# Kernel tuning notes

Hardware: AMD Instinct MI355X
Metric: run time of the kernel (lower is better)

## Reference

```python
import jax, jax.numpy as jnp
import numpy as np

N_ENTITIES = 100000
N_USERS = 50000
N_FACTORS = 4
N_RELATIONS = 32
N_META = 8
CHANNEL = 64
N_EDGES = 1600000
NNZ = 1000000


def setup_inputs() -> dict:
    key = jax.random.key(0)
    ks = jax.random.split(key, 12)
    return {
        "entity_emb": jax.random.normal(ks[0], (N_ENTITIES, CHANNEL), jnp.float32) * 0.1,
        "user_emb": jax.random.normal(ks[1], (N_USERS, CHANNEL), jnp.float32) * 0.1,
        "latent_emb": jax.random.normal(ks[2], (N_FACTORS, CHANNEL), jnp.float32) * 0.1,
        "head": jax.random.randint(ks[3], (N_EDGES,), 0, N_ENTITIES, jnp.int32),
        "tail": jax.random.randint(ks[4], (N_EDGES,), 0, N_ENTITIES, jnp.int32),
        # edge_type values in [1, n_relations) so edge_type - 1 indexes (n_relations-1) rows
        "edge_type": jax.random.randint(ks[5], (N_EDGES,), 1, N_RELATIONS, jnp.int32),
        "mat_row": jax.random.randint(ks[6], (NNZ,), 0, N_USERS, jnp.int32),
        "mat_col": jax.random.randint(ks[7], (NNZ,), 0, N_ENTITIES, jnp.int32),
        "mat_val": jax.random.uniform(ks[8], (NNZ,), jnp.float32),
        "relation_edge_weight": jax.random.normal(ks[9], (N_RELATIONS - 1, CHANNEL), jnp.float32) * 0.1,
        "weight": jax.random.normal(ks[10], (N_META, CHANNEL), jnp.float32) * 0.1,
        "disen_weight_att": jax.random.normal(ks[11], (N_FACTORS, N_META), jnp.float32) * 0.1,
    }


def reference(entity_emb, user_emb, latent_emb, head, tail, edge_type,
              mat_row, mat_col, mat_val, relation_edge_weight, weight,
              disen_weight_att):
    n_entities, channel = entity_emb.shape
    n_users = user_emb.shape[0]

    # --- KG aggregation: GATED_ATT + INDEPENDENT_RELATION_EMB branch ---
    edge_rel = relation_edge_weight[edge_type - 1]                     # (E, C)
    att = jax.nn.sigmoid(jnp.sum(entity_emb[head] * edge_rel, axis=1)) # (E,)
    neigh = att[:, None] * (entity_emb[tail] * edge_rel)               # (E, C)
    seg_sum = jax.ops.segment_sum(neigh, head, num_segments=n_entities)
    cnt = jax.ops.segment_sum(jnp.ones((head.shape[0],), entity_emb.dtype),
                              head, num_segments=n_entities)
    entity_agg = seg_sum / jnp.maximum(cnt, 1.0)[:, None]              # scatter_mean

    # --- user aggregation ---
    score = jax.nn.softmax(user_emb @ latent_emb.T, axis=1)[:, :, None]  # (U, F, 1)
    # sparse mm: interact_mat (U x N_ent, COO) @ entity_emb
    user_agg = jax.ops.segment_sum(mat_val[:, None] * entity_emb[mat_col],
                                   mat_row, num_segments=n_users)        # (U, C)
    disen_weight = jax.nn.softmax(disen_weight_att, axis=-1) @ weight    # (F, C)
    user_agg = user_agg * (disen_weight[None, :, :] * score).sum(axis=1) + user_agg
    return entity_agg, user_agg
```

## Files before the change

kernel.cpp:

```cpp
#include <hip/hip_runtime.h>

constexpr int N_ENTITIES = 100000;
constexpr int N_USERS    = 50000;
constexpr int N_FACTORS  = 4;
constexpr int N_META     = 8;
constexpr int CHANNEL    = 64;
constexpr int N_EDGES    = 1600000;
constexpr int NNZ        = 1000000;

__device__ __forceinline__ float wave_reduce_sum(float v) {
    for (int off = 32; off > 0; off >>= 1)
        v += __shfl_xor(v, off, 64);
    return v;
}

__global__ void edge_kernel(const float* __restrict__ entity_emb,
                            const int*   __restrict__ head,
                            const int*   __restrict__ tail,
                            const int*   __restrict__ etype,
                            const float* __restrict__ rel_w,
                            float*       __restrict__ ent_acc,
                            float*       __restrict__ cnt) {
    const int lane = threadIdx.x & 63;
    const int wid  = (blockIdx.x * blockDim.x + threadIdx.x) >> 6;
    const int nw   = (gridDim.x * blockDim.x) >> 6;
    for (int e = wid; e < N_EDGES; e += nw) {
        const int h = head[e];
        const int t = tail[e];
        const int r = etype[e] - 1;
        const float rw = rel_w[r * CHANNEL + lane];
        const float eh = entity_emb[h * CHANNEL + lane];
        const float dot = wave_reduce_sum(eh * rw);
        const float att = 1.0f / (1.0f + expf(-dot));
        const float et  = entity_emb[t * CHANNEL + lane];
        atomicAdd(&ent_acc[h * CHANNEL + lane], att * et * rw);
        if (lane == 0) atomicAdd(&cnt[h], 1.0f);
    }
}

__global__ void spmm_kernel(const float* __restrict__ entity_emb,
                            const int*   __restrict__ mat_row,
                            const int*   __restrict__ mat_col,
                            const float* __restrict__ mat_val,
                            float*       __restrict__ user_acc) {
    const int lane = threadIdx.x & 63;
    const int wid  = (blockIdx.x * blockDim.x + threadIdx.x) >> 6;
    const int nw   = (gridDim.x * blockDim.x) >> 6;
    for (int i = wid; i < NNZ; i += nw) {
        const int r   = mat_row[i];
        const int c   = mat_col[i];
        const float v = mat_val[i];
        const float e = entity_emb[c * CHANNEL + lane];
        atomicAdd(&user_acc[r * CHANNEL + lane], v * e);
    }
}

__global__ void ent_final_kernel(float* __restrict__ ent,
                                 const float* __restrict__ cnt) {
    const int total = N_ENTITIES * (CHANNEL / 4);
    for (int i = blockIdx.x * blockDim.x + threadIdx.x; i < total;
         i += gridDim.x * blockDim.x) {
        const int row = i >> 4;
        const float inv = 1.0f / fmaxf(cnt[row], 1.0f);
        float4 v = reinterpret_cast<float4*>(ent)[i];
        v.x *= inv; v.y *= inv; v.z *= inv; v.w *= inv;
        reinterpret_cast<float4*>(ent)[i] = v;
    }
}

__global__ void user_final_kernel(const float* __restrict__ user_emb,
                                  const float* __restrict__ latent_emb,
                                  const float* __restrict__ weight,
                                  const float* __restrict__ datt,
                                  float*       __restrict__ user_out) {
    __shared__ float dw[N_FACTORS][CHANNEL];
    const int tid = threadIdx.x;
    if (tid < N_FACTORS * CHANNEL) {
        const int f = tid >> 6, c = tid & 63;
        float m = -1e30f;
        for (int j = 0; j < N_META; ++j) m = fmaxf(m, datt[f * N_META + j]);
        float p[N_META]; float s = 0.0f;
        for (int j = 0; j < N_META; ++j) { p[j] = expf(datt[f * N_META + j] - m); s += p[j]; }
        const float invs = 1.0f / s;
        float acc = 0.0f;
        for (int j = 0; j < N_META; ++j) acc += p[j] * invs * weight[j * CHANNEL + c];
        dw[f][c] = acc;
    }
    __syncthreads();

    const int lane = tid & 63;
    const int wib  = tid >> 6;
    const int wpb  = blockDim.x >> 6;
    for (int u = blockIdx.x * wpb + wib; u < N_USERS; u += gridDim.x * wpb) {
        const float ue = user_emb[u * CHANNEL + lane];
        float d0 = wave_reduce_sum(ue * latent_emb[0 * CHANNEL + lane]);
        float d1 = wave_reduce_sum(ue * latent_emb[1 * CHANNEL + lane]);
        float d2 = wave_reduce_sum(ue * latent_emb[2 * CHANNEL + lane]);
        float d3 = wave_reduce_sum(ue * latent_emb[3 * CHANNEL + lane]);
        const float m = fmaxf(fmaxf(d0, d1), fmaxf(d2, d3));
        d0 = expf(d0 - m); d1 = expf(d1 - m); d2 = expf(d2 - m); d3 = expf(d3 - m);
        const float invs = 1.0f / (d0 + d1 + d2 + d3);
        const float g = (d0 * dw[0][lane] + d1 * dw[1][lane] +
                         d2 * dw[2][lane] + d3 * dw[3][lane]) * invs;
        const float a = user_out[u * CHANNEL + lane];
        user_out[u * CHANNEL + lane] = a * (1.0f + g);
    }
}

extern "C" void kernel_launch(void* const* d_in, const int* in_sizes, int n_in,
                              void* d_out, int out_size, void* d_ws, size_t ws_size,
                              hipStream_t stream) {
    const float* entity_emb = (const float*)d_in[0];
    const float* user_emb   = (const float*)d_in[1];
    const float* latent_emb = (const float*)d_in[2];
    const int*   head       = (const int*)d_in[3];
    const int*   tail       = (const int*)d_in[4];
    const int*   etype      = (const int*)d_in[5];
    const int*   mat_row    = (const int*)d_in[6];
    const int*   mat_col    = (const int*)d_in[7];
    const float* mat_val    = (const float*)d_in[8];
    const float* rel_w      = (const float*)d_in[9];
    const float* weight     = (const float*)d_in[10];
    const float* datt       = (const float*)d_in[11];

    float* out      = (float*)d_out;
    float* ent_acc  = out;
    float* user_acc = out + (size_t)N_ENTITIES * CHANNEL;
    float* cnt      = (float*)d_ws;

    hipMemsetAsync(d_out, 0, (size_t)out_size * sizeof(float), stream);
    hipMemsetAsync(d_ws, 0, (size_t)N_ENTITIES * sizeof(float), stream);

    edge_kernel<<<4096, 256, 0, stream>>>(entity_emb, head, tail, etype, rel_w,
                                          ent_acc, cnt);
    spmm_kernel<<<4096, 256, 0, stream>>>(entity_emb, mat_row, mat_col, mat_val,
                                          user_acc);
    ent_final_kernel<<<2048, 256, 0, stream>>>(ent_acc, cnt);
    user_final_kernel<<<1024, 256, 0, stream>>>(user_emb, latent_emb, weight,
                                                datt, user_acc);
}
```

Measured before the change: 769.7 us.

## Replace atomic scatter aggregation with counting-sort CSR gather per entity and user

Builds CSR groupings of KG edges by head and of interaction nonzeros by user via count, scan, and scatter kernels, then computes each output row with one wave gathering its neighbors. This removes per-channel float atomics, output memsets and separate finalization passes, fusing the mean and user gating into the gather kernels. It adds index-sort passes with integer atomics and a serial single-block scan, and relies on a large workspace and on bit-packing tail and relation into one int.

```diff
diff --git a/kernel.cpp b/kernel.cpp
--- a/kernel.cpp
+++ b/kernel.cpp
@@ -7,6 +7,8 @@
 constexpr int CHANNEL    = 64;
 constexpr int N_EDGES    = 1600000;
 constexpr int NNZ        = 1000000;
+constexpr int N_REL      = 31;
+
 
 __device__ __forceinline__ float wave_reduce_sum(float v) {
     for (int off = 32; off > 0; off >>= 1)
@@ -14,65 +16,114 @@
     return v;
 }
 
-__global__ void edge_kernel(const float* __restrict__ entity_emb,
-                            const int*   __restrict__ head,
-                            const int*   __restrict__ tail,
-                            const int*   __restrict__ etype,
-                            const float* __restrict__ rel_w,
-                            float*       __restrict__ ent_acc,
-                            float*       __restrict__ cnt) {
-    const int lane = threadIdx.x & 63;
-    const int wid  = (blockIdx.x * blockDim.x + threadIdx.x) >> 6;
-    const int nw   = (gridDim.x * blockDim.x) >> 6;
-    for (int e = wid; e < N_EDGES; e += nw) {
+__global__ void count_kernel(const int* __restrict__ head,
+                             const int* __restrict__ mat_row,
+                             int* __restrict__ ent_cnt,
+                             int* __restrict__ user_cnt) {
+    const int i0 = blockIdx.x * blockDim.x + threadIdx.x;
+    const int stride = gridDim.x * blockDim.x;
+    for (int e = i0; e < N_EDGES; e += stride)
+        atomicAdd(&ent_cnt[head[e]], 1);
+    for (int z = i0; z < NNZ; z += stride)
+        atomicAdd(&user_cnt[mat_row[z]], 1);
+}
+
+__global__ void scan_kernel(const int* __restrict__ ent_cnt, int* __restrict__ ent_cur,
+                            const int* __restrict__ user_cnt, int* __restrict__ user_cur) {
+    const int* cnt = (blockIdx.x == 0) ? ent_cnt : user_cnt;
+    int*       cur = (blockIdx.x == 0) ? ent_cur : user_cur;
+    const int  n   = (blockIdx.x == 0) ? N_ENTITIES : N_USERS;
+    __shared__ int partial[1024];
+    const int per   = (n + 1023) >> 10;
+    const int start = threadIdx.x * per;
+    const int end   = min(start + per, n);
+    int s = 0;
+    for (int i = start; i < end; ++i) s += cnt[i];
+    partial[threadIdx.x] = s;
+    __syncthreads();
+    for (int d = 1; d < 1024; d <<= 1) {
+        int v = (threadIdx.x >= d) ? partial[threadIdx.x - d] : 0;
+        __syncthreads();
+        partial[threadIdx.x] += v;
+        __syncthreads();
+    }
+    int base = (threadIdx.x == 0) ? 0 : partial[threadIdx.x - 1];
+    for (int i = start; i < end; ++i) {
+        cur[i] = base;
+        base += cnt[i];
+    }
+}
+
+__global__ void scatter_kernel(const int* __restrict__ head,
+                               const int* __restrict__ tail,
+                               const int* __restrict__ etype,
+                               const int* __restrict__ mat_row,
+                               const int* __restrict__ mat_col,
+                               const float* __restrict__ mat_val,
+                               int* __restrict__ ent_cur,
+                               int* __restrict__ user_cur,
+                               int* __restrict__ edge_pl,
+                               int* __restrict__ nnz_col,
+                               float* __restrict__ nnz_val) {
+    const int i0 = blockIdx.x * blockDim.x + threadIdx.x;
+    const int stride = gridDim.x * blockDim.x;
+    for (int e = i0; e < N_EDGES; e += stride) {
         const int h = head[e];
-        const int t = tail[e];
-        const int r = etype[e] - 1;
-        const float rw = rel_w[r * CHANNEL + lane];
-        const float eh = entity_emb[h * CHANNEL + lane];
-        const float dot = wave_reduce_sum(eh * rw);
-        const float att = 1.0f / (1.0f + expf(-dot));
-        const float et  = entity_emb[t * CHANNEL + lane];
-        atomicAdd(&ent_acc[h * CHANNEL + lane], att * et * rw);
-        if (lane == 0) atomicAdd(&cnt[h], 1.0f);
-    }
-}
-
-__global__ void spmm_kernel(const float* __restrict__ entity_emb,
-                            const int*   __restrict__ mat_row,
-                            const int*   __restrict__ mat_col,
-                            const float* __restrict__ mat_val,
-                            float*       __restrict__ user_acc) {
-    const int lane = threadIdx.x & 63;
-    const int wid  = (blockIdx.x * blockDim.x + threadIdx.x) >> 6;
-    const int nw   = (gridDim.x * blockDim.x) >> 6;
-    for (int i = wid; i < NNZ; i += nw) {
-        const int r   = mat_row[i];
-        const int c   = mat_col[i];
-        const float v = mat_val[i];
-        const float e = entity_emb[c * CHANNEL + lane];
-        atomicAdd(&user_acc[r * CHANNEL + lane], v * e);
-    }
-}
-
-__global__ void ent_final_kernel(float* __restrict__ ent,
-                                 const float* __restrict__ cnt) {
-    const int total = N_ENTITIES * (CHANNEL / 4);
-    for (int i = blockIdx.x * blockDim.x + threadIdx.x; i < total;
-         i += gridDim.x * blockDim.x) {
-        const int row = i >> 4;
-        const float inv = 1.0f / fmaxf(cnt[row], 1.0f);
-        float4 v = reinterpret_cast<float4*>(ent)[i];
-        v.x *= inv; v.y *= inv; v.z *= inv; v.w *= inv;
-        reinterpret_cast<float4*>(ent)[i] = v;
-    }
-}
-
-__global__ void user_final_kernel(const float* __restrict__ user_emb,
-                                  const float* __restrict__ latent_emb,
-                                  const float* __restrict__ weight,
-                                  const float* __restrict__ datt,
-                                  float*       __restrict__ user_out) {
+        const int pos = atomicAdd(&ent_cur[h], 1);
+        edge_pl[pos] = tail[e] | ((etype[e] - 1) << 17);
+    }
+    for (int z = i0; z < NNZ; z += stride) {
+        const int r = mat_row[z];
+        const int pos = atomicAdd(&user_cur[r], 1);
+        nnz_col[pos] = mat_col[z];
+        nnz_val[pos] = mat_val[z];
+    }
+}
+
+__global__ void ent_agg_kernel(const float* __restrict__ entity_emb,
+                               const float* __restrict__ rel_w,
+                               const int* __restrict__ ent_cnt,
+                               const int* __restrict__ ent_cur,
+                               const int* __restrict__ edge_pl,
+                               float* __restrict__ out_ent) {
+    __shared__ float rw_s[N_REL][CHANNEL];
+    const int tid = threadIdx.x;
+    for (int i = tid; i < N_REL * CHANNEL; i += blockDim.x)
+        rw_s[i >> 6][i & 63] = rel_w[i];
+    __syncthreads();
+
+    const int lane = tid & 63;
+    const int wib  = tid >> 6;
+    const int wpb  = blockDim.x >> 6;
+    for (int h = blockIdx.x * wpb + wib; h < N_ENTITIES; h += gridDim.x * wpb) {
+        const int cnt   = ent_cnt[h];
+        const int end   = ent_cur[h];
+        const int start = end - cnt;
+        const float eh  = entity_emb[h * CHANNEL + lane];
+        float acc = 0.0f;
+        for (int i = start; i < end; ++i) {
+            const int pl = edge_pl[i];
+            const int t  = pl & 0x1FFFF;
+            const int r  = pl >> 17;
+            const float rw = rw_s[r][lane];
+            const float d  = wave_reduce_sum(eh * rw);
+            const float att = 1.0f / (1.0f + __expf(-d));
+            acc += att * rw * entity_emb[t * CHANNEL + lane];
+        }
+        out_ent[h * CHANNEL + lane] = acc / fmaxf((float)cnt, 1.0f);
+    }
+}
+
+__global__ void user_agg_kernel(const float* __restrict__ entity_emb,
+                                const float* __restrict__ user_emb,
+                                const float* __restrict__ latent_emb,
+                                const float* __restrict__ weight,
+                                const float* __restrict__ datt,
+                                const int* __restrict__ user_cnt,
+                                const int* __restrict__ user_cur,
+                                const int* __restrict__ nnz_col,
+                                const float* __restrict__ nnz_val,
+                                float* __restrict__ out_user) {
     __shared__ float dw[N_FACTORS][CHANNEL];
     const int tid = threadIdx.x;
     if (tid < N_FACTORS * CHANNEL) {
@@ -80,7 +131,7 @@
         float m = -1e30f;
         for (int j = 0; j < N_META; ++j) m = fmaxf(m, datt[f * N_META + j]);
         float p[N_META]; float s = 0.0f;
-        for (int j = 0; j < N_META; ++j) { p[j] = expf(datt[f * N_META + j] - m); s += p[j]; }
+        for (int j = 0; j < N_META; ++j) { p[j] = __expf(datt[f * N_META + j] - m); s += p[j]; }
         const float invs = 1.0f / s;
         float acc = 0.0f;
         for (int j = 0; j < N_META; ++j) acc += p[j] * invs * weight[j * CHANNEL + c];
@@ -92,18 +143,27 @@
     const int wib  = tid >> 6;
     const int wpb  = blockDim.x >> 6;
     for (int u = blockIdx.x * wpb + wib; u < N_USERS; u += gridDim.x * wpb) {
+        const int cnt   = user_cnt[u];
+        const int end   = user_cur[u];
+        const int start = end - cnt;
+        float acc = 0.0f;
+        for (int i = start; i < end; ++i) {
+            const int c   = nnz_col[i];
+            const float v = nnz_val[i];
+            acc += v * entity_emb[c * CHANNEL + lane];
+        }
         const float ue = user_emb[u * CHANNEL + lane];
         float d0 = wave_reduce_sum(ue * latent_emb[0 * CHANNEL + lane]);
         float d1 = wave_reduce_sum(ue * latent_emb[1 * CHANNEL + lane]);
         float d2 = wave_reduce_sum(ue * latent_emb[2 * CHANNEL + lane]);
         float d3 = wave_reduce_sum(ue * latent_emb[3 * CHANNEL + lane]);
         const float m = fmaxf(fmaxf(d0, d1), fmaxf(d2, d3));
-        d0 = expf(d0 - m); d1 = expf(d1 - m); d2 = expf(d2 - m); d3 = expf(d3 - m);
+        d0 = __expf(d0 - m); d1 = __expf(d1 - m);
+        d2 = __expf(d2 - m); d3 = __expf(d3 - m);
         const float invs = 1.0f / (d0 + d1 + d2 + d3);
         const float g = (d0 * dw[0][lane] + d1 * dw[1][lane] +
                          d2 * dw[2][lane] + d3 * dw[3][lane]) * invs;
-        const float a = user_out[u * CHANNEL + lane];
-        user_out[u * CHANNEL + lane] = a * (1.0f + g);
+        out_user[u * CHANNEL + lane] = acc * (1.0f + g);
     }
 }
 
@@ -124,18 +184,28 @@
     const float* datt       = (const float*)d_in[11];
 
     float* out      = (float*)d_out;
-    float* ent_acc  = out;
-    float* user_acc = out + (size_t)N_ENTITIES * CHANNEL;
-    float* cnt      = (float*)d_ws;
-
-    hipMemsetAsync(d_out, 0, (size_t)out_size * sizeof(float), stream);
-    hipMemsetAsync(d_ws, 0, (size_t)N_ENTITIES * sizeof(float), stream);
-
-    edge_kernel<<<4096, 256, 0, stream>>>(entity_emb, head, tail, etype, rel_w,
-                                          ent_acc, cnt);
-    spmm_kernel<<<4096, 256, 0, stream>>>(entity_emb, mat_row, mat_col, mat_val,
-                                          user_acc);
-    ent_final_kernel<<<2048, 256, 0, stream>>>(ent_acc, cnt);
-    user_final_kernel<<<1024, 256, 0, stream>>>(user_emb, latent_emb, weight,
-                                                datt, user_acc);
-}
+    float* out_ent  = out;
+    float* out_user = out + (size_t)N_ENTITIES * CHANNEL;
+
+    int*   ws       = (int*)d_ws;
+    int*   ent_cnt  = ws;
+    int*   user_cnt = ws + 100000;
+    int*   ent_cur  = ws + 150000;
+    int*   user_cur = ws + 250000;
+    int*   edge_pl  = ws + 300000;
+    int*   nnz_col  = ws + 1900000;
+    float* nnz_val  = (float*)(ws + 2900000);
+
+    hipMemsetAsync(ent_cnt, 0, 150000 * sizeof(int), stream);
+
+    count_kernel<<<2048, 256, 0, stream>>>(head, mat_row, ent_cnt, user_cnt);
+    scan_kernel<<<2, 1024, 0, stream>>>(ent_cnt, ent_cur, user_cnt, user_cur);
+    scatter_kernel<<<2048, 256, 0, stream>>>(head, tail, etype, mat_row, mat_col,
+                                             mat_val, ent_cur, user_cur,
+                                             edge_pl, nnz_col, nnz_val);
+    ent_agg_kernel<<<4096, 256, 0, stream>>>(entity_emb, rel_w, ent_cnt, ent_cur,
+                                             edge_pl, out_ent);
+    user_agg_kernel<<<2048, 256, 0, stream>>>(entity_emb, user_emb, latent_emb,
+                                              weight, datt, user_cnt, user_cur,
+                                              nnz_col, nnz_val, out_user);
+}
```

Measured after the change: 833.1 us. +8.2%, slower.

## Bucket edges by destination and accumulate in shared memory instead of global atomics

Applied to the files above, without the earlier changes.

Replaces the per-edge global atomic scatter with a counting-sort pipeline: a histogram, a scan, and a scatter pack edges and nonzeros into coarse destination buckets. Aggregation blocks then accumulate into shared memory and write each output row once. Attention is precomputed per (head, relation) pair in shared memory, and the mean and user gating are fused into the aggregation kernels. This removes heavy global float atomics and the separate finalize passes, but adds preprocessing passes, extra payload traffic, and redundant payload scans across the four sub-blocks of each bucket.

```diff
diff --git a/kernel.cpp b/kernel.cpp
--- a/kernel.cpp
+++ b/kernel.cpp
@@ -7,6 +7,13 @@
 constexpr int CHANNEL    = 64;
 constexpr int N_EDGES    = 1600000;
 constexpr int NNZ        = 1000000;
+constexpr int N_REL      = 31;
+
+constexpr int CB   = 196;
+constexpr int TILE = 8192;
+constexpr int ETILES = (N_EDGES + TILE - 1) / TILE;
+constexpr int NTILES = (NNZ + TILE - 1) / TILE;
+
 
 __device__ __forceinline__ float wave_reduce_sum(float v) {
     for (int off = 32; off > 0; off >>= 1)
@@ -14,96 +21,193 @@
     return v;
 }
 
-__global__ void edge_kernel(const float* __restrict__ entity_emb,
-                            const int*   __restrict__ head,
-                            const int*   __restrict__ tail,
-                            const int*   __restrict__ etype,
-                            const float* __restrict__ rel_w,
-                            float*       __restrict__ ent_acc,
-                            float*       __restrict__ cnt) {
-    const int lane = threadIdx.x & 63;
-    const int wid  = (blockIdx.x * blockDim.x + threadIdx.x) >> 6;
-    const int nw   = (gridDim.x * blockDim.x) >> 6;
-    for (int e = wid; e < N_EDGES; e += nw) {
-        const int h = head[e];
-        const int t = tail[e];
-        const int r = etype[e] - 1;
-        const float rw = rel_w[r * CHANNEL + lane];
-        const float eh = entity_emb[h * CHANNEL + lane];
-        const float dot = wave_reduce_sum(eh * rw);
-        const float att = 1.0f / (1.0f + expf(-dot));
-        const float et  = entity_emb[t * CHANNEL + lane];
-        atomicAdd(&ent_acc[h * CHANNEL + lane], att * et * rw);
-        if (lane == 0) atomicAdd(&cnt[h], 1.0f);
-    }
-}
-
-__global__ void spmm_kernel(const float* __restrict__ entity_emb,
-                            const int*   __restrict__ mat_row,
-                            const int*   __restrict__ mat_col,
-                            const float* __restrict__ mat_val,
-                            float*       __restrict__ user_acc) {
-    const int lane = threadIdx.x & 63;
-    const int wid  = (blockIdx.x * blockDim.x + threadIdx.x) >> 6;
-    const int nw   = (gridDim.x * blockDim.x) >> 6;
-    for (int i = wid; i < NNZ; i += nw) {
-        const int r   = mat_row[i];
-        const int c   = mat_col[i];
-        const float v = mat_val[i];
-        const float e = entity_emb[c * CHANNEL + lane];
-        atomicAdd(&user_acc[r * CHANNEL + lane], v * e);
-    }
-}
-
-__global__ void ent_final_kernel(float* __restrict__ ent,
-                                 const float* __restrict__ cnt) {
-    const int total = N_ENTITIES * (CHANNEL / 4);
-    for (int i = blockIdx.x * blockDim.x + threadIdx.x; i < total;
-         i += gridDim.x * blockDim.x) {
-        const int row = i >> 4;
-        const float inv = 1.0f / fmaxf(cnt[row], 1.0f);
-        float4 v = reinterpret_cast<float4*>(ent)[i];
-        v.x *= inv; v.y *= inv; v.z *= inv; v.w *= inv;
-        reinterpret_cast<float4*>(ent)[i] = v;
-    }
-}
-
-__global__ void user_final_kernel(const float* __restrict__ user_emb,
-                                  const float* __restrict__ latent_emb,
-                                  const float* __restrict__ weight,
-                                  const float* __restrict__ datt,
-                                  float*       __restrict__ user_out) {
+__global__ void count_kernel(const int* __restrict__ head,
+                             const int* __restrict__ mat_row,
+                             int* __restrict__ cnt_e, int* __restrict__ cnt_n) {
+    __shared__ int he[CB], hn[CB];
+    for (int i = threadIdx.x; i < CB; i += blockDim.x) { he[i] = 0; hn[i] = 0; }
+    __syncthreads();
+    const int i0 = blockIdx.x * blockDim.x + threadIdx.x;
+    const int st = gridDim.x * blockDim.x;
+    for (int e = i0; e < N_EDGES; e += st) atomicAdd(&he[head[e] >> 9], 1);
+    for (int z = i0; z < NNZ;     z += st) atomicAdd(&hn[mat_row[z] >> 8], 1);
+    __syncthreads();
+    for (int i = threadIdx.x; i < CB; i += blockDim.x) {
+        if (he[i]) atomicAdd(&cnt_e[i], he[i]);
+        if (hn[i]) atomicAdd(&cnt_n[i], hn[i]);
+    }
+}
+
+__global__ void scan_kernel(const int* __restrict__ cnt_e, const int* __restrict__ cnt_n,
+                            int* __restrict__ base_e, int* __restrict__ base_n,
+                            int* __restrict__ cur_e, int* __restrict__ cur_n) {
+    if (threadIdx.x == 0) {
+        int s = 0;
+        for (int i = 0; i < CB; ++i) { base_e[i] = s; cur_e[i] = s; s += cnt_e[i]; }
+        base_e[CB] = s;
+    }
+    if (threadIdx.x == 1) {
+        int s = 0;
+        for (int i = 0; i < CB; ++i) { base_n[i] = s; cur_n[i] = s; s += cnt_n[i]; }
+        base_n[CB] = s;
+    }
+}
+
+__global__ void scatter_kernel(const int* __restrict__ head,
+                               const int* __restrict__ tail,
+                               const int* __restrict__ etype,
+                               const int* __restrict__ mat_row,
+                               const int* __restrict__ mat_col,
+                               const float* __restrict__ mat_val,
+                               int* __restrict__ cur_e, int* __restrict__ cur_n,
+                               int* __restrict__ pay_e, int2* __restrict__ pay_n) {
+    __shared__ int hist[CB], bbase[CB], lcur[CB];
+    const int tid = threadIdx.x;
+    for (int i = tid; i < CB; i += blockDim.x) { hist[i] = 0; lcur[i] = 0; }
+    __syncthreads();
+    if (blockIdx.x < ETILES) {
+        const int s = blockIdx.x * TILE, e = min(s + TILE, N_EDGES);
+        for (int i = s + tid; i < e; i += blockDim.x) atomicAdd(&hist[head[i] >> 9], 1);
+        __syncthreads();
+        for (int b = tid; b < CB; b += blockDim.x)
+            if (hist[b]) bbase[b] = atomicAdd(&cur_e[b], hist[b]);
+        __syncthreads();
+        for (int i = s + tid; i < e; i += blockDim.x) {
+            const int h = head[i], b = h >> 9;
+            const int pos = atomicAdd(&lcur[b], 1);
+            pay_e[bbase[b] + pos] = ((h & 511) << 22) | ((etype[i] - 1) << 17) | tail[i];
+        }
+    } else {
+        const int s = (blockIdx.x - ETILES) * TILE, e = min(s + TILE, NNZ);
+        for (int i = s + tid; i < e; i += blockDim.x) atomicAdd(&hist[mat_row[i] >> 8], 1);
+        __syncthreads();
+        for (int b = tid; b < CB; b += blockDim.x)
+            if (hist[b]) bbase[b] = atomicAdd(&cur_n[b], hist[b]);
+        __syncthreads();
+        for (int i = s + tid; i < e; i += blockDim.x) {
+            const int r = mat_row[i], b = r >> 8;
+            const int pos = atomicAdd(&lcur[b], 1);
+            int2 p; p.x = ((r & 255) << 17) | mat_col[i]; p.y = __float_as_int(mat_val[i]);
+            pay_n[bbase[b] + pos] = p;
+        }
+    }
+}
+
+__global__ void ent_agg_kernel(const float* __restrict__ emb,
+                               const float* __restrict__ rel_w,
+                               const int* __restrict__ base_e,
+                               const int* __restrict__ cnt_e,
+                               const int* __restrict__ pay_e,
+                               float* __restrict__ out_ent) {
+    __shared__ float accum[128][CHANNEL];
+    __shared__ float att_s[128][N_REL];
+    __shared__ int   cnt_s[128];
+    const int tid = threadIdx.x;
+    const int cb  = blockIdx.x >> 2, sub = blockIdx.x & 3;
+    const int h0  = cb * 512 + sub * 128;
+
+    for (int i = tid; i < 128 * CHANNEL; i += 256) accum[i >> 6][i & 63] = 0.f;
+    if (tid < 128) cnt_s[tid] = 0;
+    for (int p = tid; p < 128 * 32; p += 256) {
+        const int hl = p >> 5, r = p & 31;
+        if (r < N_REL) {
+            const int h = h0 + hl;
+            float a = 0.f;
+            if (h < N_ENTITIES) {
+                for (int c = 0; c < CHANNEL; ++c)
+                    a += emb[h * CHANNEL + c] * rel_w[r * CHANNEL + c];
+                a = 1.f / (1.f + __expf(-a));
+            }
+            att_s[hl][r] = a;
+        }
+    }
+    __syncthreads();
+
+    const int lane = tid & 63, wib = tid >> 6;
+    const int start = base_e[cb], end = start + cnt_e[cb];
+    for (int i = start + wib * 64; i < end; i += 4 * 64) {
+        const int idx = i + lane;
+        const int pl = (idx < end) ? pay_e[idx] : 0;
+        const bool mine = (idx < end) && (((pl >> 29) & 3) == sub);
+        unsigned long long m = __ballot(mine);
+        while (m) {
+            const int b = __ffsll((long long)m) - 1; m &= m - 1;
+            const int p  = __shfl(pl, b);
+            const int hl = (p >> 22) & 127, r = (p >> 17) & 31, t = p & 0x1FFFF;
+            const float contrib = att_s[hl][r] * rel_w[r * CHANNEL + lane] *
+                                  emb[t * CHANNEL + lane];
+            atomicAdd(&accum[hl][lane], contrib);
+            if (lane == 0) atomicAdd(&cnt_s[hl], 1);
+        }
+    }
+    __syncthreads();
+    for (int hl = wib; hl < 128; hl += 4) {
+        const int h = h0 + hl;
+        if (h < N_ENTITIES)
+            out_ent[h * CHANNEL + lane] = accum[hl][lane] / fmaxf((float)cnt_s[hl], 1.f);
+    }
+}
+
+__global__ void user_agg_kernel(const float* __restrict__ emb,
+                                const float* __restrict__ user_emb,
+                                const float* __restrict__ latent,
+                                const float* __restrict__ weight,
+                                const float* __restrict__ datt,
+                                const int* __restrict__ base_n,
+                                const int* __restrict__ cnt_n,
+                                const int2* __restrict__ pay_n,
+                                float* __restrict__ out_user) {
+    __shared__ float accum[64][CHANNEL];
     __shared__ float dw[N_FACTORS][CHANNEL];
     const int tid = threadIdx.x;
-    if (tid < N_FACTORS * CHANNEL) {
+    const int cb  = blockIdx.x >> 2, sub = blockIdx.x & 3;
+    const int u0  = cb * 256 + sub * 64;
+
+    for (int i = tid; i < 64 * CHANNEL; i += 256) accum[i >> 6][i & 63] = 0.f;
+    {
         const int f = tid >> 6, c = tid & 63;
-        float m = -1e30f;
-        for (int j = 0; j < N_META; ++j) m = fmaxf(m, datt[f * N_META + j]);
-        float p[N_META]; float s = 0.0f;
-        for (int j = 0; j < N_META; ++j) { p[j] = expf(datt[f * N_META + j] - m); s += p[j]; }
-        const float invs = 1.0f / s;
-        float acc = 0.0f;
-        for (int j = 0; j < N_META; ++j) acc += p[j] * invs * weight[j * CHANNEL + c];
-        dw[f][c] = acc;
-    }
-    __syncthreads();
-
-    const int lane = tid & 63;
-    const int wib  = tid >> 6;
-    const int wpb  = blockDim.x >> 6;
-    for (int u = blockIdx.x * wpb + wib; u < N_USERS; u += gridDim.x * wpb) {
-        const float ue = user_emb[u * CHANNEL + lane];
-        float d0 = wave_reduce_sum(ue * latent_emb[0 * CHANNEL + lane]);
-        float d1 = wave_reduce_sum(ue * latent_emb[1 * CHANNEL + lane]);
-        float d2 = wave_reduce_sum(ue * latent_emb[2 * CHANNEL + lane]);
-        float d3 = wave_reduce_sum(ue * latent_emb[3 * CHANNEL + lane]);
-        const float m = fmaxf(fmaxf(d0, d1), fmaxf(d2, d3));
-        d0 = expf(d0 - m); d1 = expf(d1 - m); d2 = expf(d2 - m); d3 = expf(d3 - m);
-        const float invs = 1.0f / (d0 + d1 + d2 + d3);
-        const float g = (d0 * dw[0][lane] + d1 * dw[1][lane] +
-                         d2 * dw[2][lane] + d3 * dw[3][lane]) * invs;
-        const float a = user_out[u * CHANNEL + lane];
-        user_out[u * CHANNEL + lane] = a * (1.0f + g);
+        float mx = -1e30f;
+        for (int j = 0; j < N_META; ++j) mx = fmaxf(mx, datt[f * N_META + j]);
+        float p[N_META], s = 0.f;
+        for (int j = 0; j < N_META; ++j) { p[j] = __expf(datt[f * N_META + j] - mx); s += p[j]; }
+        float acc = 0.f;
+        for (int j = 0; j < N_META; ++j) acc += p[j] * weight[j * CHANNEL + c];
+        dw[f][c] = acc / s;
+    }
+    __syncthreads();
+
+    const int lane = tid & 63, wib = tid >> 6;
+    const int start = base_n[cb], end = start + cnt_n[cb];
+    for (int i = start + wib * 64; i < end; i += 4 * 64) {
+        const int idx = i + lane;
+        int2 pl = make_int2(0, 0);
+        if (idx < end) pl = pay_n[idx];
+        const bool mine = (idx < end) && (((pl.x >> 23) & 3) == sub);
+        unsigned long long m = __ballot(mine);
+        while (m) {
+            const int b = __ffsll((long long)m) - 1; m &= m - 1;
+            const int w0 = __shfl(pl.x, b), w1 = __shfl(pl.y, b);
+            const int ul = (w0 >> 17) & 63, c = w0 & 0x1FFFF;
+            atomicAdd(&accum[ul][lane], __int_as_float(w1) * emb[c * CHANNEL + lane]);
+        }
+    }
+    __syncthreads();
+    for (int ul = wib; ul < 64; ul += 4) {
+        const int u = u0 + ul;
+        if (u < N_USERS) {
+            const float ue = user_emb[u * CHANNEL + lane];
+            float d0 = wave_reduce_sum(ue * latent[0 * CHANNEL + lane]);
+            float d1 = wave_reduce_sum(ue * latent[1 * CHANNEL + lane]);
+            float d2 = wave_reduce_sum(ue * latent[2 * CHANNEL + lane]);
+            float d3 = wave_reduce_sum(ue * latent[3 * CHANNEL + lane]);
+            const float mx = fmaxf(fmaxf(d0, d1), fmaxf(d2, d3));
+            d0 = __expf(d0 - mx); d1 = __expf(d1 - mx);
+            d2 = __expf(d2 - mx); d3 = __expf(d3 - mx);
+            const float invs = 1.f / (d0 + d1 + d2 + d3);
+            const float g = (d0 * dw[0][lane] + d1 * dw[1][lane] +
+                             d2 * dw[2][lane] + d3 * dw[3][lane]) * invs;
+            out_user[u * CHANNEL + lane] = accum[ul][lane] * (1.f + g);
+        }
     }
 }
 
@@ -124,18 +228,29 @@
     const float* datt       = (const float*)d_in[11];
 
     float* out      = (float*)d_out;
-    float* ent_acc  = out;
-    float* user_acc = out + (size_t)N_ENTITIES * CHANNEL;
-    float* cnt      = (float*)d_ws;
-
-    hipMemsetAsync(d_out, 0, (size_t)out_size * sizeof(float), stream);
-    hipMemsetAsync(d_ws, 0, (size_t)N_ENTITIES * sizeof(float), stream);
-
-    edge_kernel<<<4096, 256, 0, stream>>>(entity_emb, head, tail, etype, rel_w,
-                                          ent_acc, cnt);
-    spmm_kernel<<<4096, 256, 0, stream>>>(entity_emb, mat_row, mat_col, mat_val,
-                                          user_acc);
-    ent_final_kernel<<<2048, 256, 0, stream>>>(ent_acc, cnt);
-    user_final_kernel<<<1024, 256, 0, stream>>>(user_emb, latent_emb, weight,
-                                                datt, user_acc);
-}
+    float* out_ent  = out;
+    float* out_user = out + (size_t)N_ENTITIES * CHANNEL;
+
+    int*  ws     = (int*)d_ws;
+    int*  cnt_e  = ws;
+    int*  cnt_n  = ws + 200;
+    int*  base_e = ws + 400;
+    int*  base_n = ws + 600;
+    int*  cur_e  = ws + 800;
+    int*  cur_n  = ws + 1000;
+    int*  pay_e  = ws + 1280;
+    int2* pay_n  = (int2*)(ws + 1601280);
+
+    hipMemsetAsync(ws, 0, 400 * sizeof(int), stream);
+
+    count_kernel<<<256, 256, 0, stream>>>(head, mat_row, cnt_e, cnt_n);
+    scan_kernel<<<1, 64, 0, stream>>>(cnt_e, cnt_n, base_e, base_n, cur_e, cur_n);
+    scatter_kernel<<<ETILES + NTILES, 256, 0, stream>>>(head, tail, etype,
+                                                        mat_row, mat_col, mat_val,
+                                                        cur_e, cur_n, pay_e, pay_n);
+    ent_agg_kernel<<<784, 256, 0, stream>>>(entity_emb, rel_w, base_e, cnt_e,
+                                            pay_e, out_ent);
+    user_agg_kernel<<<784, 256, 0, stream>>>(entity_emb, user_emb, latent_emb,
+                                             weight, datt, base_n, cnt_n,
+                                             pay_n, out_user);
+}
```

Result: slower. 1.579 ms (+105.1%).
